# Performance work log

Hardware: AMD Instinct MI355X
Metric: run time of the kernel (lower is better)

The kernel has to match this reference:

```python
import jax, jax.numpy as jnp
import numpy as np

ALPHA = 0.5
WIN_SIZE = 31
BN_EPS = 1e-5
LRELU_SLOPE = 0.1


def setup_inputs() -> dict:
    key = jax.random.key(0)
    k1, k2, k3, k4 = jax.random.split(key, 4)
    B, N, C, P, E = 4, 2048, 64, 48, 128
    return {
        "sig_new": jax.random.normal(k1, (B, N, C, P), dtype=jnp.float32),
        "atten_mem": jax.random.normal(k2, (B, N, C, P), dtype=jnp.float32),
        "conv_w": jax.random.normal(k3, (E, C, P), dtype=jnp.float32) * 0.05,
        "conv_b": jax.random.normal(k4, (E,), dtype=jnp.float32) * 0.05,
        "bn_gamma": jnp.ones((E,), dtype=jnp.float32),
        "bn_beta": jnp.zeros((E,), dtype=jnp.float32),
    }


def _neighbour_mask(n_cutout):
    # clamped banded mask (pano_scan=False / training-mode branch)
    half = WIN_SIZE // 2
    cols = jnp.clip(jnp.arange(n_cutout)[:, None] + jnp.arange(-half, half + 1)[None, :], 0, n_cutout - 1)
    rows = jnp.broadcast_to(jnp.arange(n_cutout)[:, None], cols.shape)
    return jnp.zeros((n_cutout, n_cutout), jnp.float32).at[rows, cols].set(1.0)


def _embed(x, conv_w, conv_b, bn_gamma, bn_beta, B, N):
    # Conv1d(kernel=n_pts) on length-n_pts input == full contraction over (c, p)
    y = jnp.einsum("ncp,ecp->ne", x.reshape(-1, x.shape[-2], x.shape[-1]), conv_w) + conv_b
    # BatchNorm1d, training-mode batch statistics over the (B*N) batch dim
    mu = y.mean(axis=0)
    var = ((y - mu) ** 2).mean(axis=0)
    y = (y - mu) * jax.lax.rsqrt(var + BN_EPS) * bn_gamma + bn_beta
    y = jnp.where(y >= 0, y, LRELU_SLOPE * y)  # LeakyReLU(0.1)
    return y.reshape(B, N, -1)


def reference(sig_new, atten_mem, conv_w, conv_b, bn_gamma, bn_beta):
    B, N, C, P = sig_new.shape
    mask = _neighbour_mask(N)
    embed_x = _embed(sig_new, conv_w, conv_b, bn_gamma, bn_beta, B, N)      # [B,N,E]
    embed_t = _embed(atten_mem, conv_w, conv_b, bn_gamma, bn_beta, B, N)    # [B,N,E]
    sim = jnp.einsum("bie,bje->bij", embed_x, embed_t)                      # [B,N,N]
    sim = sim - 1e10 * (1.0 - mask)
    mx = jnp.max(sim, axis=-1, keepdims=True)
    ex = jnp.exp(sim - mx) * mask
    attn = ex / jnp.sum(ex, axis=-1, keepdims=True)                          # [B,N,N]
    mem_flat = atten_mem.reshape(B, N, C * P)
    mem_w = jnp.einsum("bij,bjf->bif", attn, mem_flat).reshape(B, N, C, P)
    new_mem = ALPHA * sig_new + (1.0 - ALPHA) * mem_w
    return new_mem, attn
```

## Files before the change

### kernel.cpp

```cpp
#include <hip/hip_runtime.h>

#define BATCH 4
#define NDIM 2048
#define EDIM 128
#define KDIM 3072
#define MDIM 8192
#define HALF 15

typedef __attribute__((ext_vector_type(8))) short short8v;
typedef __attribute__((ext_vector_type(4))) float f32x4;

__device__ inline ushort bf16h(float x) {
  union { float f; unsigned u; } v; v.f = x;
  unsigned r = v.u + 0x7fff + ((v.u >> 16) & 1);
  return (ushort)(r >> 16);
}

__global__ __launch_bounds__(256)
void k_wprep(const float* __restrict__ w, ushort* __restrict__ wh, ushort* __restrict__ wl) {
  const int q = (blockIdx.x * 256 + threadIdx.x) * 4;
  float4 v = *(const float4*)(w + q);
  const float f[4] = {v.x, v.y, v.z, v.w};
  ushort4 h, l;
  ushort* ph = (ushort*)&h; ushort* pl = (ushort*)&l;
#pragma unroll
  for (int j = 0; j < 4; ++j) {
    unsigned u = __float_as_uint(f[j]);
    ph[j] = (ushort)(u >> 16);
    pl[j] = bf16h(f[j] - __uint_as_float(u & 0xffff0000u));
  }
  *(ushort4*)(wh + q) = h;
  *(ushort4*)(wl + q) = l;
}

#define BMT 64
#define BK 32

__global__ __launch_bounds__(256, 4)
void k_gemm(const float* __restrict__ x0, const float* __restrict__ x1,
            const ushort* __restrict__ wh, const ushort* __restrict__ wl,
            float* __restrict__ part, int splitK) {
  const int tid = threadIdx.x;
  const int m0 = blockIdx.x * BMT;
  const int kc = blockIdx.y;
  const int inp = blockIdx.z;
  const float* __restrict__ x = inp ? x1 : x0;
  const int kpc = KDIM / splitK;
  const int kbeg = kc * kpc;
  const int nsteps = kpc / BK;

  __shared__ ushort sAh[BMT][BK];
  __shared__ ushort sAl[BMT][BK];
  __shared__ ushort sBh[EDIM][BK];
  __shared__ ushort sBl[EDIM][BK];

  const int mrow = tid >> 3;
  const int c4 = (tid & 7) << 2;

  const int lane = tid & 63;
  const int wid = tid >> 6;
  const int wr = wid >> 1;
  const int wc = wid & 1;
  const int fr = lane & 15;
  const int kg = (lane >> 4) << 3;

  f32x4 acc[2][4];
#pragma unroll
  for (int a = 0; a < 2; ++a)
#pragma unroll
    for (int b = 0; b < 4; ++b) acc[a][b] = (f32x4){0.f, 0.f, 0.f, 0.f};

  float4 rA[2];
  ushort4 rBh[4], rBl[4];
  {
    const float* xb = x + (size_t)(m0 + mrow) * KDIM + kbeg + c4;
    const ushort* wb = wh + (size_t)mrow * KDIM + kbeg + c4;
    const ushort* wb2 = wl + (size_t)mrow * KDIM + kbeg + c4;
#pragma unroll
    for (int i = 0; i < 2; ++i)
      rA[i] = *(const float4*)(xb + (size_t)(32 * i) * KDIM);
#pragma unroll
    for (int i = 0; i < 4; ++i) {
      rBh[i] = *(const ushort4*)(wb + (size_t)(32 * i) * KDIM);
      rBl[i] = *(const ushort4*)(wb2 + (size_t)(32 * i) * KDIM);
    }
  }

  for (int st = 0; st < nsteps; ++st) {
    __syncthreads();
#pragma unroll
    for (int i = 0; i < 2; ++i) {
      const int m = mrow + 32 * i;
      const float fa[4] = {rA[i].x, rA[i].y, rA[i].z, rA[i].w};
      ushort4 ah, al;
      ushort* pah = (ushort*)&ah; ushort* pal = (ushort*)&al;
#pragma unroll
      for (int j = 0; j < 4; ++j) {
        unsigned u = __float_as_uint(fa[j]);
        pah[j] = (ushort)(u >> 16);
        pal[j] = bf16h(fa[j] - __uint_as_float(u & 0xffff0000u));
      }
      *(ushort4*)&sAh[m][c4] = ah;
      *(ushort4*)&sAl[m][c4] = al;
    }
#pragma unroll
    for (int i = 0; i < 4; ++i) {
      const int m = mrow + 32 * i;
      *(ushort4*)&sBh[m][c4] = rBh[i];
      *(ushort4*)&sBl[m][c4] = rBl[i];
    }
    __syncthreads();

    if (st + 1 < nsteps) {
      const int ko = kbeg + (st + 1) * BK + c4;
      const float* xb = x + (size_t)(m0 + mrow) * KDIM + ko;
      const ushort* wb = wh + (size_t)mrow * KDIM + ko;
      const ushort* wb2 = wl + (size_t)mrow * KDIM + ko;
#pragma unroll
      for (int i = 0; i < 2; ++i)
        rA[i] = *(const float4*)(xb + (size_t)(32 * i) * KDIM);
#pragma unroll
      for (int i = 0; i < 4; ++i) {
        rBh[i] = *(const ushort4*)(wb + (size_t)(32 * i) * KDIM);
        rBl[i] = *(const ushort4*)(wb2 + (size_t)(32 * i) * KDIM);
      }
    }

    short8v ah[2], al[2], bh[4], bl[4];
#pragma unroll
    for (int mi = 0; mi < 2; ++mi) {
      const int row = wr * 32 + mi * 16 + fr;
      ah[mi] = *(const short8v*)&sAh[row][kg];
      al[mi] = *(const short8v*)&sAl[row][kg];
    }
#pragma unroll
    for (int ei = 0; ei < 4; ++ei) {
      const int e = wc * 64 + ei * 16 + fr;
      bh[ei] = *(const short8v*)&sBh[e][kg];
      bl[ei] = *(const short8v*)&sBl[e][kg];
    }
#pragma unroll
    for (int mi = 0; mi < 2; ++mi)
#pragma unroll
      for (int ei = 0; ei < 4; ++ei) {
        acc[mi][ei] = __builtin_amdgcn_mfma_f32_16x16x32_bf16(ah[mi], bh[ei], acc[mi][ei], 0, 0, 0);
        acc[mi][ei] = __builtin_amdgcn_mfma_f32_16x16x32_bf16(ah[mi], bl[ei], acc[mi][ei], 0, 0, 0);
        acc[mi][ei] = __builtin_amdgcn_mfma_f32_16x16x32_bf16(al[mi], bh[ei], acc[mi][ei], 0, 0, 0);
      }
  }

  float* po = part + ((size_t)(inp * splitK + kc) * MDIM + m0) * EDIM;
#pragma unroll
  for (int mi = 0; mi < 2; ++mi) {
    const int mloc = wr * 32 + mi * 16 + ((lane >> 4) << 2);
#pragma unroll
    for (int ei = 0; ei < 4; ++ei) {
      const int e = wc * 64 + ei * 16 + fr;
#pragma unroll
      for (int r = 0; r < 4; ++r)
        po[(size_t)(mloc + r) * EDIM + e] = acc[mi][ei][r];
    }
  }
}

__global__ __launch_bounds__(256)
void k_reduce(const float* __restrict__ part, const float* __restrict__ bvec,
              float* __restrict__ y, float* __restrict__ spart, int splitK) {
  const int tid = threadIdx.x;
  const int in = blockIdx.z;
  const int rb = blockIdx.x;
  const int e = tid & 127;
  const int rh = tid >> 7;
  const float bb = bvec[e];
  float s = 0.f, s2 = 0.f;
  for (int rr = 0; rr < 32; ++rr) {
    const int r = rb * 64 + rh * 32 + rr;
    float v = 0.f;
    for (int kc = 0; kc < splitK; ++kc)
      v += part[((size_t)(in * splitK + kc) * MDIM + r) * EDIM + e];
    v += bb;
    y[((size_t)in * MDIM + r) * EDIM + e] = v;
    s += v; s2 += v * v;
  }
  __shared__ float l1[256], l2[256];
  l1[tid] = s; l2[tid] = s2;
  __syncthreads();
  if (rh == 0) {
    s = l1[e] + l1[e + 128];
    s2 = l2[e] + l2[e + 128];
    spart[((size_t)(in * 128 + rb) * 2 + 0) * 128 + e] = s;
    spart[((size_t)(in * 128 + rb) * 2 + 1) * 128 + e] = s2;
  }
}

__global__ void k_finalize(const float* __restrict__ spart, const float* __restrict__ gamma,
                           const float* __restrict__ beta, float* __restrict__ scsh) {
  const int in = blockIdx.x;
  const int e = threadIdx.x;
  float s = 0.f, s2 = 0.f;
  for (int rb = 0; rb < 128; ++rb) {
    s  += spart[((size_t)(in * 128 + rb) * 2 + 0) * 128 + e];
    s2 += spart[((size_t)(in * 128 + rb) * 2 + 1) * 128 + e];
  }
  const float mu = s * (1.f / MDIM);
  const float var = s2 * (1.f / MDIM) - mu * mu;
  const float rs = rsqrtf(var + 1e-5f);
  const float sc = gamma[e] * rs;
  const float sh = beta[e] - mu * sc;
  scsh[in * 128 + e] = sc;
  scsh[256 + in * 128 + e] = sh;
}

#define SIMW 34
#define SIMP 132

__global__ __launch_bounds__(256)
void k_sim(const float* __restrict__ y, const float* __restrict__ scsh,
           float* __restrict__ attn, float* __restrict__ aw) {
  const int tid = threadIdx.x;
  const int bid = blockIdx.x;
  const int b = bid >> 9;
  const int i0 = (bid << 2) & 2047;
  const int jlo = max(0, i0 - HALF);
  const int jhi = min(NDIM - 1, i0 + 3 + HALF);
  const int tw = jhi - jlo + 1;

  __shared__ float sT[SIMW][SIMP];
  __shared__ float sX[4][SIMP];
  __shared__ float sSc[2][128], sSh[2][128];

  if (tid < 128) { sSc[0][tid] = scsh[tid]; sSh[0][tid] = scsh[256 + tid]; }
  else { const int e = tid - 128; sSc[1][e] = scsh[128 + e]; sSh[1][e] = scsh[384 + e]; }
  __syncthreads();

  const int totq = (4 + tw) * 32;
  for (int q = tid; q < totq; q += 256) {
    const int rr = q >> 5;
    const int e4 = (q & 31) << 2;
    const bool isx = rr < 4;
    const int gr = isx ? ((b << 11) + i0 + rr)
                       : (MDIM + (b << 11) + jlo + (rr - 4));
    float4 v = *(const float4*)(y + (size_t)gr * EDIM + e4);
    const float* sc = isx ? sSc[0] : sSc[1];
    const float* sh = isx ? sSh[0] : sSh[1];
    const float* pv = (const float*)&v;
    float* dst = isx ? &sX[rr][e4] : &sT[rr - 4][e4];
#pragma unroll
    for (int t = 0; t < 4; ++t) {
      const float val = fmaf(sc[e4 + t], pv[t], sh[e4 + t]);
      dst[t] = val >= 0.f ? val : 0.1f * val;
    }
  }
  __syncthreads();

  const int lane = tid & 63;
  const int wv = tid >> 6;
  const int i = i0 + wv;
  const int row = (b << 11) + i;
  const int jliw = max(0, i - HALF);
  const int jhiw = min(NDIM - 1, i + HALF);
  const int j = jliw + lane;
  const bool valid = (lane < 31) && (j <= jhiw);
  const int trow = (valid ? j : jliw) - jlo;

  float s = 0.f;
#pragma unroll
  for (int e = 0; e < EDIM; e += 4) {
    float4 u = *(const float4*)&sX[wv][e];
    float4 v = *(const float4*)&sT[trow][e];
    s = fmaf(u.x, v.x, s); s = fmaf(u.y, v.y, s);
    s = fmaf(u.z, v.z, s); s = fmaf(u.w, v.w, s);
  }
  float sm = valid ? s : -1e30f;
  float mx = sm;
#pragma unroll
  for (int o = 1; o < 64; o <<= 1) mx = fmaxf(mx, __shfl_xor(mx, o));
  const float p = valid ? __expf(sm - mx) : 0.f;
  float ss = p;
#pragma unroll
  for (int o = 1; o < 64; o <<= 1) ss += __shfl_xor(ss, o);
  const float a = p / ss;

  float* orow = attn + (size_t)row * NDIM;
  const int bw = jhiw - jliw;
  for (int c0 = lane << 2; c0 < NDIM; c0 += 256) {
    float4 v;
    float* pv = (float*)&v;
#pragma unroll
    for (int t = 0; t < 4; ++t) {
      const int d = c0 + t - jliw;
      const float val = __shfl(a, d & 63);
      pv[t] = (d >= 0 && d <= bw) ? val : 0.f;
    }
    *(float4*)(orow + c0) = v;
  }
  if (lane < 32) aw[(size_t)row * 32 + lane] = valid ? a : 0.f;
}

#define TI 16
#define TJMAX 46
#define FC 256
#define NIT (NDIM / TI)
#define NFC (KDIM / FC)
#define NWG_MEMW (NIT * NFC * BATCH)

__global__ __launch_bounds__(256, 2)
void k_memw(const float* __restrict__ sig, const float* __restrict__ mem,
            const float* __restrict__ aw, float* __restrict__ out) {
  const int tid = threadIdx.x;
  const int bid = blockIdx.x;
  const int nid = (bid & 7) * (NWG_MEMW / 8) + (bid >> 3);
  const int b  = nid / (NIT * NFC);
  const int r  = nid % (NIT * NFC);
  const int fc0 = (r / NIT) * FC;
  const int i0  = (r % NIT) * TI;
  const int jlo = max(0, i0 - HALF);
  const int jhi = min(NDIM - 1, i0 + TI - 1 + HALF);
  const int tj = jhi - jlo + 1;

  __shared__ float sV[TJMAX][FC];
  __shared__ float sWt[TJMAX][TI];

  for (int idx = tid; idx < tj * TI; idx += 256) {
    const int jj = idx >> 4;
    const int ii = idx & 15;
    const int ii_g = i0 + ii;
    const int jg = jlo + jj;
    const int jli = max(0, ii_g - HALF);
    const int jhii = min(NDIM - 1, ii_g + HALF);
    float wv = 0.f;
    if (jg >= jli && jg <= jhii) wv = aw[(size_t)((b << 11) + ii_g) * 32 + (jg - jli)];
    sWt[jj][ii] = wv;
  }
  for (int idx = tid; idx < tj * (FC / 4); idx += 256) {
    const int jj = idx >> 6;
    const int f4 = idx & 63;
    *(float4*)&sV[jj][f4 << 2] =
        *(const float4*)(mem + (size_t)((b << 11) + jlo + jj) * KDIM + fc0 + (f4 << 2));
  }
  __syncthreads();

  const int ig = tid >> 6;
  const int fg = tid & 63;
  const int ibase = i0 + (ig << 2);
  const int wlo = max(jlo, ibase - HALF) - jlo;
  const int whi = min(jhi, ibase + 3 + HALF) - jlo;

  float acc[4][4];
#pragma unroll
  for (int a = 0; a < 4; ++a)
#pragma unroll
    for (int c = 0; c < 4; ++c) acc[a][c] = 0.f;

  for (int jj = wlo; jj <= whi; ++jj) {
    float4 wv = *(const float4*)&sWt[jj][ig << 2];
    float4 vv = *(const float4*)&sV[jj][fg << 2];
    const float wa[4] = {wv.x, wv.y, wv.z, wv.w};
    const float va[4] = {vv.x, vv.y, vv.z, vv.w};
#pragma unroll
    for (int mi = 0; mi < 4; ++mi)
#pragma unroll
      for (int fi = 0; fi < 4; ++fi)
        acc[mi][fi] = fmaf(wa[mi], va[fi], acc[mi][fi]);
  }

  const size_t base = (size_t)((b << 11) + ibase) * KDIM + fc0 + (fg << 2);
#pragma unroll
  for (int mi = 0; mi < 4; ++mi) {
    float4 sv = *(const float4*)(sig + base + (size_t)mi * KDIM);
    float4 ov;
    ov.x = 0.5f * sv.x + 0.5f * acc[mi][0];
    ov.y = 0.5f * sv.y + 0.5f * acc[mi][1];
    ov.z = 0.5f * sv.z + 0.5f * acc[mi][2];
    ov.w = 0.5f * sv.w + 0.5f * acc[mi][3];
    *(float4*)(out + base + (size_t)mi * KDIM) = ov;
  }
}

extern "C" void kernel_launch(void* const* d_in, const int* in_sizes, int n_in,
                              void* d_out, int out_size, void* d_ws, size_t ws_size,
                              hipStream_t stream) {
  const float* sig   = (const float*)d_in[0];
  const float* mem   = (const float*)d_in[1];
  const float* w     = (const float*)d_in[2];
  const float* bv    = (const float*)d_in[3];
  const float* gamma = (const float*)d_in[4];
  const float* beta  = (const float*)d_in[5];

  float* out_mem  = (float*)d_out;
  float* out_attn = out_mem + (size_t)BATCH * NDIM * KDIM;

  float* wsf = (float*)d_ws;
  const size_t ME = (size_t)MDIM * EDIM;
  const size_t fixed = 2 * ME + 65536 + 512 + 262144 + 196608;
  int splitK = 4;
  while (splitK > 1 && ((size_t)2 * splitK * ME + fixed) * 4 > ws_size) splitK >>= 1;

  float* part  = wsf;
  float* y     = part + (size_t)2 * splitK * ME;
  float* spart = y + 2 * ME;
  float* scsh  = spart + 65536;
  float* aw    = scsh + 512;
  ushort* wh   = (ushort*)(aw + 262144);
  ushort* wl   = wh + (size_t)EDIM * KDIM;

  hipLaunchKernelGGL(k_wprep, dim3(EDIM * KDIM / 1024), dim3(256), 0, stream, w, wh, wl);

  dim3 g1(MDIM / BMT, splitK, 2);
  hipLaunchKernelGGL(k_gemm, g1, dim3(256), 0, stream, sig, mem, wh, wl, part, splitK);

  dim3 g2(MDIM / 64, 1, 2);
  hipLaunchKernelGGL(k_reduce, g2, dim3(256), 0, stream, part, bv, y, spart, splitK);

  hipLaunchKernelGGL(k_finalize, dim3(2), dim3(128), 0, stream, spart, gamma, beta, scsh);

  hipLaunchKernelGGL(k_sim, dim3(MDIM / 4), dim3(256), 0, stream, y, scsh, out_attn, aw);

  hipLaunchKernelGGL(k_memw, dim3(NWG_MEMW), dim3(256), 0, stream, sig, mem, aw, out_mem);
}
```

Measured before the change: 474.0 us.

## Enlarge GEMM tiles with swizzled LDS and loop feature chunks in memw blocks

The embedding GEMM moves from 64x32 to 128x64 tiles, with 4x4 MFMA fragments per wave and an XOR-swizzled shared-memory layout to avoid bank conflicts; launch bounds drop to 2 waves per SIMD. The memw kernel now launches one block per 16-row tile and loops over all feature chunks, reloading the attention weights once per block instead of once per chunk. The aim is more reuse per load and fewer LDS conflicts in the GEMM. The cost is less occupancy and parallelism, and memw has far fewer blocks (512) doing serial chunk loops with extra barriers.

New measurement: 469.9 us. About the same (-0.9%).

```diff
diff --git a/kernel.cpp b/kernel.cpp
--- a/kernel.cpp
+++ b/kernel.cpp
@@ -33,10 +33,11 @@
   *(ushort4*)(wl + q) = l;
 }
 
-#define BMT 64
-#define BK 32
-
-__global__ __launch_bounds__(256, 4)
+#define BMT 128
+#define BK 64
+#define SWZ(row, k) (((row) << 6) + (((((k) >> 3) ^ ((row) & 7)) << 3) | ((k) & 7)))
+
+__global__ __launch_bounds__(256, 2)
 void k_gemm(const float* __restrict__ x0, const float* __restrict__ x1,
             const ushort* __restrict__ wh, const ushort* __restrict__ wl,
             float* __restrict__ part, int splitK) {
@@ -49,13 +50,13 @@
   const int kbeg = kc * kpc;
   const int nsteps = kpc / BK;
 
-  __shared__ ushort sAh[BMT][BK];
-  __shared__ ushort sAl[BMT][BK];
-  __shared__ ushort sBh[EDIM][BK];
-  __shared__ ushort sBl[EDIM][BK];
-
-  const int mrow = tid >> 3;
-  const int c4 = (tid & 7) << 2;
+  __shared__ ushort sAh[BMT * BK];
+  __shared__ ushort sAl[BMT * BK];
+  __shared__ ushort sBh[EDIM * BK];
+  __shared__ ushort sBl[EDIM * BK];
+
+  const int srow = tid >> 2;
+  const int skb = (tid & 3) << 4;
 
   const int lane = tid & 63;
   const int wid = tid >> 6;
@@ -64,95 +65,99 @@
   const int fr = lane & 15;
   const int kg = (lane >> 4) << 3;
 
-  f32x4 acc[2][4];
-#pragma unroll
-  for (int a = 0; a < 2; ++a)
+  f32x4 acc[4][4];
+#pragma unroll
+  for (int a = 0; a < 4; ++a)
 #pragma unroll
     for (int b = 0; b < 4; ++b) acc[a][b] = (f32x4){0.f, 0.f, 0.f, 0.f};
 
-  float4 rA[2];
-  ushort4 rBh[4], rBl[4];
+  float4 rA[2][4];
+  ushort4 rBh[2][4], rBl[2][4];
   {
-    const float* xb = x + (size_t)(m0 + mrow) * KDIM + kbeg + c4;
-    const ushort* wb = wh + (size_t)mrow * KDIM + kbeg + c4;
-    const ushort* wb2 = wl + (size_t)mrow * KDIM + kbeg + c4;
-#pragma unroll
-    for (int i = 0; i < 2; ++i)
-      rA[i] = *(const float4*)(xb + (size_t)(32 * i) * KDIM);
-#pragma unroll
-    for (int i = 0; i < 4; ++i) {
-      rBh[i] = *(const ushort4*)(wb + (size_t)(32 * i) * KDIM);
-      rBl[i] = *(const ushort4*)(wb2 + (size_t)(32 * i) * KDIM);
-    }
+    const float* xb = x + (size_t)(m0 + srow) * KDIM + kbeg + skb;
+    const ushort* wb = wh + (size_t)srow * KDIM + kbeg + skb;
+    const ushort* wb2 = wl + (size_t)srow * KDIM + kbeg + skb;
+#pragma unroll
+    for (int h = 0; h < 2; ++h)
+#pragma unroll
+      for (int j = 0; j < 4; ++j) {
+        rA[h][j]  = *(const float4*)(xb + (size_t)(64 * h) * KDIM + 4 * j);
+        rBh[h][j] = *(const ushort4*)(wb + (size_t)(64 * h) * KDIM + 4 * j);
+        rBl[h][j] = *(const ushort4*)(wb2 + (size_t)(64 * h) * KDIM + 4 * j);
+      }
   }
 
   for (int st = 0; st < nsteps; ++st) {
     __syncthreads();
 #pragma unroll
-    for (int i = 0; i < 2; ++i) {
-      const int m = mrow + 32 * i;
-      const float fa[4] = {rA[i].x, rA[i].y, rA[i].z, rA[i].w};
-      ushort4 ah, al;
-      ushort* pah = (ushort*)&ah; ushort* pal = (ushort*)&al;
+    for (int h = 0; h < 2; ++h) {
+      const int row = srow + 64 * h;
 #pragma unroll
       for (int j = 0; j < 4; ++j) {
-        unsigned u = __float_as_uint(fa[j]);
-        pah[j] = (ushort)(u >> 16);
-        pal[j] = bf16h(fa[j] - __uint_as_float(u & 0xffff0000u));
+        const int k = skb + 4 * j;
+        const float fa[4] = {rA[h][j].x, rA[h][j].y, rA[h][j].z, rA[h][j].w};
+        ushort4 ah, al;
+        ushort* pah = (ushort*)&ah; ushort* pal = (ushort*)&al;
+#pragma unroll
+        for (int t = 0; t < 4; ++t) {
+          unsigned u = __float_as_uint(fa[t]);
+          pah[t] = (ushort)(u >> 16);
+          pal[t] = bf16h(fa[t] - __uint_as_float(u & 0xffff0000u));
+        }
+        *(ushort4*)&sAh[SWZ(row, k)] = ah;
+        *(ushort4*)&sAl[SWZ(row, k)] = al;
+        *(ushort4*)&sBh[SWZ(row, k)] = rBh[h][j];
+        *(ushort4*)&sBl[SWZ(row, k)] = rBl[h][j];
       }
-      *(ushort4*)&sAh[m][c4] = ah;
-      *(ushort4*)&sAl[m][c4] = al;
-    }
-#pragma unroll
-    for (int i = 0; i < 4; ++i) {
-      const int m = mrow + 32 * i;
-      *(ushort4*)&sBh[m][c4] = rBh[i];
-      *(ushort4*)&sBl[m][c4] = rBl[i];
     }
     __syncthreads();
 
     if (st + 1 < nsteps) {
-      const int ko = kbeg + (st + 1) * BK + c4;
-      const float* xb = x + (size_t)(m0 + mrow) * KDIM + ko;
-      const ushort* wb = wh + (size_t)mrow * KDIM + ko;
-      const ushort* wb2 = wl + (size_t)mrow * KDIM + ko;
-#pragma unroll
-      for (int i = 0; i < 2; ++i)
-        rA[i] = *(const float4*)(xb + (size_t)(32 * i) * KDIM);
-#pragma unroll
-      for (int i = 0; i < 4; ++i) {
-        rBh[i] = *(const ushort4*)(wb + (size_t)(32 * i) * KDIM);
-        rBl[i] = *(const ushort4*)(wb2 + (size_t)(32 * i) * KDIM);
+      const int ko = kbeg + (st + 1) * BK + skb;
+      const float* xb = x + (size_t)(m0 + srow) * KDIM + ko;
+      const ushort* wb = wh + (size_t)srow * KDIM + ko;
+      const ushort* wb2 = wl + (size_t)srow * KDIM + ko;
+#pragma unroll
+      for (int h = 0; h < 2; ++h)
+#pragma unroll
+        for (int j = 0; j < 4; ++j) {
+          rA[h][j]  = *(const float4*)(xb + (size_t)(64 * h) * KDIM + 4 * j);
+          rBh[h][j] = *(const ushort4*)(wb + (size_t)(64 * h) * KDIM + 4 * j);
+          rBl[h][j] = *(const ushort4*)(wb2 + (size_t)(64 * h) * KDIM + 4 * j);
+        }
+    }
+
+#pragma unroll
+    for (int kk = 0; kk < 2; ++kk) {
+      const int kb2 = kg + 32 * kk;
+      short8v ah[4], al[4], bh[4], bl[4];
+#pragma unroll
+      for (int mi = 0; mi < 4; ++mi) {
+        const int row = wr * 64 + mi * 16 + fr;
+        ah[mi] = *(const short8v*)&sAh[SWZ(row, kb2)];
+        al[mi] = *(const short8v*)&sAl[SWZ(row, kb2)];
       }
-    }
-
-    short8v ah[2], al[2], bh[4], bl[4];
-#pragma unroll
-    for (int mi = 0; mi < 2; ++mi) {
-      const int row = wr * 32 + mi * 16 + fr;
-      ah[mi] = *(const short8v*)&sAh[row][kg];
-      al[mi] = *(const short8v*)&sAl[row][kg];
-    }
-#pragma unroll
-    for (int ei = 0; ei < 4; ++ei) {
-      const int e = wc * 64 + ei * 16 + fr;
-      bh[ei] = *(const short8v*)&sBh[e][kg];
-      bl[ei] = *(const short8v*)&sBl[e][kg];
-    }
-#pragma unroll
-    for (int mi = 0; mi < 2; ++mi)
 #pragma unroll
       for (int ei = 0; ei < 4; ++ei) {
-        acc[mi][ei] = __builtin_amdgcn_mfma_f32_16x16x32_bf16(ah[mi], bh[ei], acc[mi][ei], 0, 0, 0);
-        acc[mi][ei] = __builtin_amdgcn_mfma_f32_16x16x32_bf16(ah[mi], bl[ei], acc[mi][ei], 0, 0, 0);
-        acc[mi][ei] = __builtin_amdgcn_mfma_f32_16x16x32_bf16(al[mi], bh[ei], acc[mi][ei], 0, 0, 0);
+        const int e = wc * 64 + ei * 16 + fr;
+        bh[ei] = *(const short8v*)&sBh[SWZ(e, kb2)];
+        bl[ei] = *(const short8v*)&sBl[SWZ(e, kb2)];
       }
+#pragma unroll
+      for (int mi = 0; mi < 4; ++mi)
+#pragma unroll
+        for (int ei = 0; ei < 4; ++ei) {
+          acc[mi][ei] = __builtin_amdgcn_mfma_f32_16x16x32_bf16(ah[mi], bh[ei], acc[mi][ei], 0, 0, 0);
+          acc[mi][ei] = __builtin_amdgcn_mfma_f32_16x16x32_bf16(ah[mi], bl[ei], acc[mi][ei], 0, 0, 0);
+          acc[mi][ei] = __builtin_amdgcn_mfma_f32_16x16x32_bf16(al[mi], bh[ei], acc[mi][ei], 0, 0, 0);
+        }
+    }
   }
 
   float* po = part + ((size_t)(inp * splitK + kc) * MDIM + m0) * EDIM;
 #pragma unroll
-  for (int mi = 0; mi < 2; ++mi) {
-    const int mloc = wr * 32 + mi * 16 + ((lane >> 4) << 2);
+  for (int mi = 0; mi < 4; ++mi) {
+    const int mloc = wr * 64 + mi * 16 + ((lane >> 4) << 2);
 #pragma unroll
     for (int ei = 0; ei < 4; ++ei) {
       const int e = wc * 64 + ei * 16 + fr;
@@ -299,26 +304,22 @@
 
 #define TI 16
 #define TJMAX 46
-#define FC 256
-#define NIT (NDIM / TI)
-#define NFC (KDIM / FC)
-#define NWG_MEMW (NIT * NFC * BATCH)
+#define FCW 256
+#define NWG2 (NDIM / TI * BATCH)
 
 __global__ __launch_bounds__(256, 2)
 void k_memw(const float* __restrict__ sig, const float* __restrict__ mem,
             const float* __restrict__ aw, float* __restrict__ out) {
   const int tid = threadIdx.x;
   const int bid = blockIdx.x;
-  const int nid = (bid & 7) * (NWG_MEMW / 8) + (bid >> 3);
-  const int b  = nid / (NIT * NFC);
-  const int r  = nid % (NIT * NFC);
-  const int fc0 = (r / NIT) * FC;
-  const int i0  = (r % NIT) * TI;
+  const int nid = (bid & 7) * (NWG2 / 8) + (bid >> 3);
+  const int b = nid >> 7;
+  const int i0 = (nid & 127) << 4;
   const int jlo = max(0, i0 - HALF);
   const int jhi = min(NDIM - 1, i0 + TI - 1 + HALF);
   const int tj = jhi - jlo + 1;
 
-  __shared__ float sV[TJMAX][FC];
+  __shared__ float sV[TJMAX][FCW];
   __shared__ float sWt[TJMAX][TI];
 
   for (int idx = tid; idx < tj * TI; idx += 256) {
@@ -332,13 +333,6 @@
     if (jg >= jli && jg <= jhii) wv = aw[(size_t)((b << 11) + ii_g) * 32 + (jg - jli)];
     sWt[jj][ii] = wv;
   }
-  for (int idx = tid; idx < tj * (FC / 4); idx += 256) {
-    const int jj = idx >> 6;
-    const int f4 = idx & 63;
-    *(float4*)&sV[jj][f4 << 2] =
-        *(const float4*)(mem + (size_t)((b << 11) + jlo + jj) * KDIM + fc0 + (f4 << 2));
-  }
-  __syncthreads();
 
   const int ig = tid >> 6;
   const int fg = tid & 63;
@@ -346,34 +340,45 @@
   const int wlo = max(jlo, ibase - HALF) - jlo;
   const int whi = min(jhi, ibase + 3 + HALF) - jlo;
 
-  float acc[4][4];
-#pragma unroll
-  for (int a = 0; a < 4; ++a)
-#pragma unroll
-    for (int c = 0; c < 4; ++c) acc[a][c] = 0.f;
-
-  for (int jj = wlo; jj <= whi; ++jj) {
-    float4 wv = *(const float4*)&sWt[jj][ig << 2];
-    float4 vv = *(const float4*)&sV[jj][fg << 2];
-    const float wa[4] = {wv.x, wv.y, wv.z, wv.w};
-    const float va[4] = {vv.x, vv.y, vv.z, vv.w};
-#pragma unroll
-    for (int mi = 0; mi < 4; ++mi)
-#pragma unroll
-      for (int fi = 0; fi < 4; ++fi)
-        acc[mi][fi] = fmaf(wa[mi], va[fi], acc[mi][fi]);
-  }
-
-  const size_t base = (size_t)((b << 11) + ibase) * KDIM + fc0 + (fg << 2);
-#pragma unroll
-  for (int mi = 0; mi < 4; ++mi) {
-    float4 sv = *(const float4*)(sig + base + (size_t)mi * KDIM);
-    float4 ov;
-    ov.x = 0.5f * sv.x + 0.5f * acc[mi][0];
-    ov.y = 0.5f * sv.y + 0.5f * acc[mi][1];
-    ov.z = 0.5f * sv.z + 0.5f * acc[mi][2];
-    ov.w = 0.5f * sv.w + 0.5f * acc[mi][3];
-    *(float4*)(out + base + (size_t)mi * KDIM) = ov;
+  for (int fc0 = 0; fc0 < KDIM; fc0 += FCW) {
+    for (int idx = tid; idx < tj * (FCW / 4); idx += 256) {
+      const int jj = idx >> 6;
+      const int f4 = idx & 63;
+      *(float4*)&sV[jj][f4 << 2] =
+          *(const float4*)(mem + (size_t)((b << 11) + jlo + jj) * KDIM + fc0 + (f4 << 2));
+    }
+    __syncthreads();
+
+    float acc[4][4];
+#pragma unroll
+    for (int a = 0; a < 4; ++a)
+#pragma unroll
+      for (int c = 0; c < 4; ++c) acc[a][c] = 0.f;
+
+    for (int jj = wlo; jj <= whi; ++jj) {
+      float4 wv = *(const float4*)&sWt[jj][ig << 2];
+      float4 vv = *(const float4*)&sV[jj][fg << 2];
+      const float wa[4] = {wv.x, wv.y, wv.z, wv.w};
+      const float va[4] = {vv.x, vv.y, vv.z, vv.w};
+#pragma unroll
+      for (int mi = 0; mi < 4; ++mi)
+#pragma unroll
+        for (int fi = 0; fi < 4; ++fi)
+          acc[mi][fi] = fmaf(wa[mi], va[fi], acc[mi][fi]);
+    }
+
+    const size_t base = (size_t)((b << 11) + ibase) * KDIM + fc0 + (fg << 2);
+#pragma unroll
+    for (int mi = 0; mi < 4; ++mi) {
+      float4 sv = *(const float4*)(sig + base + (size_t)mi * KDIM);
+      float4 ov;
+      ov.x = 0.5f * sv.x + 0.5f * acc[mi][0];
+      ov.y = 0.5f * sv.y + 0.5f * acc[mi][1];
+      ov.z = 0.5f * sv.z + 0.5f * acc[mi][2];
+      ov.w = 0.5f * sv.w + 0.5f * acc[mi][3];
+      *(float4*)(out + base + (size_t)mi * KDIM) = ov;
+    }
+    __syncthreads();
   }
 }
 
@@ -416,5 +421,5 @@
 
   hipLaunchKernelGGL(k_sim, dim3(MDIM / 4), dim3(256), 0, stream, y, scsh, out_attn, aw);
 
-  hipLaunchKernelGGL(k_memw, dim3(NWG_MEMW), dim3(256), 0, stream, sig, mem, aw, out_mem);
-}
+  hipLaunchKernelGGL(k_memw, dim3(NWG2), dim3(256), 0, stream, sig, mem, aw, out_mem);
+}
```
